# Kernel optimization log

Measured on AMD Instinct MI355X. Metric: run time of the kernel, lower is better.

Reference implementation:

```python
import jax, jax.numpy as jnp
import numpy as np

CAPACITY = 0.5


def setup_inputs() -> dict:
    key = jax.random.key(0)
    ks = jax.random.split(key, 5)
    B, L, D = 4, 4096, 1024
    Dff = 4 * D
    x = jax.random.normal(ks[0], (B, L, D), dtype=jnp.float32)
    w_router = jax.random.normal(ks[1], (D,), dtype=jnp.float32) / np.sqrt(D)
    w_bypass = jax.random.normal(ks[2], (D, D), dtype=jnp.float32) / np.sqrt(D)
    w1 = jax.random.normal(ks[3], (Dff, D), dtype=jnp.float32) / np.sqrt(D)
    w2 = jax.random.normal(ks[4], (D, Dff), dtype=jnp.float32) / np.sqrt(Dff)
    return {"x": x, "w_router": w_router, "w_bypass": w_bypass, "w1": w1, "w2": w2}


def _block_fn(x, w1, w2):
    # stand-in for the expensive full block: 2-layer GELU FFN (torch Linear: y = x W^T)
    h = jax.nn.gelu(jnp.einsum('bld,fd->blf', x, w1))
    return jnp.einsum('blf,df->bld', h, w2)


def reference(x, w_router, w_bypass, w1, w2):
    B, L, D = x.shape
    k = max(1, int(L * CAPACITY))  # static
    if k >= L:
        return _block_fn(x, w1, w2)
    # router scores (B, L)
    scores = jnp.einsum('bld,d->bl', x, w_router)
    _, top_idx = jax.lax.top_k(scores, k)          # (B, k)
    top_idx = jnp.sort(top_idx, axis=-1)           # (B, k), sorted positions
    # gather selected tokens -> (B, k, D)
    x_sel = jnp.take_along_axis(x, top_idx[:, :, None], axis=1)
    out_sel = _block_fn(x_sel, w1, w2)             # (B, k, D)
    # bypass path for all tokens
    output = jnp.einsum('bld,ed->ble', x, w_bypass)
    # scatter block outputs back onto selected positions
    b_idx = jnp.arange(B)[:, None]                 # (B, 1)
    output = output.at[b_idx, top_idx].set(out_sel)
    return output
```

## Files before the change

### kernel.cpp

```cpp
#include <hip/hip_runtime.h>
#include <stdint.h>
#include <math.h>


typedef __attribute__((ext_vector_type(8))) __bf16 bf16x8;
typedef __attribute__((ext_vector_type(4))) float f32x4;

__device__ __forceinline__ void async_cp16(const __bf16* g, __bf16* l) {
    __builtin_amdgcn_global_load_lds(
        (__attribute__((address_space(1))) void*)g,
        (__attribute__((address_space(3))) void*)l,
        16, 0, 0);
}

__device__ __forceinline__ float gelu_fast(float x) {
    float u = 1.5957691216057308f * x * (1.0f + 0.044715f * x * x);
    return x / (1.0f + __expf(-u));
}

__global__ __launch_bounds__(256) void router_cvt(
    const float* __restrict__ x, const float* __restrict__ wr,
    float* __restrict__ scores, __bf16* __restrict__ xb)
{
    int wid  = (blockIdx.x * blockDim.x + threadIdx.x) >> 6;
    int lane = threadIdx.x & 63;
    const float* row = x + (size_t)wid * 1024;
    __bf16* orow = xb + (size_t)wid * 1024;
    double s = 0.0;
    #pragma unroll
    for (int it = 0; it < 2; ++it) {
        int base = it * 512 + lane * 8;
        float4 a  = *(const float4*)(row + base);
        float4 b  = *(const float4*)(row + base + 4);
        float4 wa = *(const float4*)(wr + base);
        float4 wc = *(const float4*)(wr + base + 4);
        s += (double)a.x * wa.x + (double)a.y * wa.y
           + (double)a.z * wa.z + (double)a.w * wa.w
           + (double)b.x * wc.x + (double)b.y * wc.y
           + (double)b.z * wc.z + (double)b.w * wc.w;
        bf16x8 v;
        v[0] = (__bf16)a.x; v[1] = (__bf16)a.y; v[2] = (__bf16)a.z; v[3] = (__bf16)a.w;
        v[4] = (__bf16)b.x; v[5] = (__bf16)b.y; v[6] = (__bf16)b.z; v[7] = (__bf16)b.w;
        *(bf16x8*)(orow + base) = v;
    }
    #pragma unroll
    for (int off = 32; off > 0; off >>= 1) s += __shfl_down(s, off, 64);
    if (lane == 0) scores[wid] = (float)s;
}

__global__ __launch_bounds__(256) void cvt3(
    const float* __restrict__ p0, const float* __restrict__ p1,
    const float* __restrict__ p2,
    __bf16* __restrict__ o0, __bf16* __restrict__ o1, __bf16* __restrict__ o2,
    int c0, int c1, int c2)
{
    int chunk = blockIdx.x * 256 + threadIdx.x;
    const float* in; __bf16* out;
    if (chunk < c0)                { in = p0 + (size_t)chunk * 8;             out = o0 + (size_t)chunk * 8; }
    else if (chunk < c0 + c1)      { int c = chunk - c0;      in = p1 + (size_t)c * 8; out = o1 + (size_t)c * 8; }
    else if (chunk < c0 + c1 + c2) { int c = chunk - c0 - c1; in = p2 + (size_t)c * 8; out = o2 + (size_t)c * 8; }
    else return;
    float4 a = *(const float4*)(in);
    float4 b = *(const float4*)(in + 4);
    bf16x8 v;
    v[0] = (__bf16)a.x; v[1] = (__bf16)a.y; v[2] = (__bf16)a.z; v[3] = (__bf16)a.w;
    v[4] = (__bf16)b.x; v[5] = (__bf16)b.y; v[6] = (__bf16)b.z; v[7] = (__bf16)b.w;
    *(bf16x8*)(out) = v;
}

__global__ __launch_bounds__(1024) void topk_build(
    const float* __restrict__ scores,
    int* __restrict__ sel_rows, int* __restrict__ byp_rows)
{
    const int L = 4096, K = 2048;
    __shared__ unsigned long long key[4096];
    __shared__ int flag[4096];
    __shared__ int tsum[1024];
    int b = blockIdx.x, t = threadIdx.x;

    for (int i = t; i < L; i += 1024) {
        unsigned u = __float_as_uint(scores[b * L + i]);
        u = (u & 0x80000000u) ? ~u : (u | 0x80000000u);
        key[i] = ((unsigned long long)u << 32) | (unsigned)(L - 1 - i);
    }
    __syncthreads();

    for (int kk = 2; kk <= L; kk <<= 1) {
        for (int j = kk >> 1; j > 0; j >>= 1) {
            for (int i = t; i < L; i += 1024) {
                int p = i ^ j;
                if (p > i) {
                    unsigned long long a = key[i], c = key[p];
                    bool sw = ((i & kk) == 0) ? (a < c) : (a > c);
                    if (sw) { key[i] = c; key[p] = a; }
                }
            }
            __syncthreads();
        }
    }

    for (int s = t; s < L; s += 1024) {
        int idx = (L - 1) - (int)(key[s] & 0xffffffffu);
        flag[idx] = (s < K) ? 1 : 0;
    }
    __syncthreads();

    int base = t * 4;
    int f0 = flag[base], f1 = flag[base+1], f2 = flag[base+2], f3 = flag[base+3];
    tsum[t] = f0 + f1 + f2 + f3;
    __syncthreads();
    for (int off = 1; off < 1024; off <<= 1) {
        int v = tsum[t];
        if (t >= off) v += tsum[t - off];
        __syncthreads();
        tsum[t] = v;
        __syncthreads();
    }
    int run = (t > 0) ? tsum[t - 1] : 0;
    int fl[4] = {f0, f1, f2, f3};
    #pragma unroll
    for (int j = 0; j < 4; ++j) {
        int idx = base + j;
        if (fl[j]) { sel_rows[b * K + run] = b * L + idx; run++; }
        else       { byp_rows[b * (L - K) + (idx - run)] = b * L + idx; }
    }
}

template <bool GATHER_A, bool SCATTER_OUT, bool GELU_ACT, typename OT>
__global__ __launch_bounds__(256) void gemm_async(
    const __bf16* __restrict__ A, const __bf16* __restrict__ W,
    OT* __restrict__ Out, const int* __restrict__ rows,
    int K, int lda, int ldo)
{
    constexpr int BM = 128, BK = 64;
    __shared__ __align__(16) __bf16 As[BM * BK];
    __shared__ __align__(16) __bf16 Bs[BM * BK];
    __shared__ int rs[BM];

    const int tid = threadIdx.x;
    const int m0 = blockIdx.y * BM, n0 = blockIdx.x * BM;
    if (tid < BM) rs[tid] = rows ? rows[m0 + tid] : (m0 + tid);
    __syncthreads();

    const int sub = tid >> 3;
    const int gc  = (tid & 7) ^ (sub & 7);
    const __bf16* aptr[4]; const __bf16* bptr[4];
    __bf16* adst[4]; __bf16* bdst[4];
    #pragma unroll
    for (int i = 0; i < 4; ++i) {
        int row = i * 32 + sub;
        int ar  = GATHER_A ? rs[row] : (m0 + row);
        aptr[i] = A + (size_t)ar * lda + gc * 8;
        bptr[i] = W + (size_t)(n0 + row) * K + gc * 8;
        adst[i] = As + (i * 256 + tid) * 8;
        bdst[i] = Bs + (i * 256 + tid) * 8;
    }

    f32x4 acc[4][4] = {};
    const int lane = tid & 63;
    const int wv = tid >> 6;
    const int wr = (wv >> 1) * 64, wc = (wv & 1) * 64;
    const int r = lane & 15, quad = lane >> 4;

    for (int k0 = 0; k0 < K; k0 += BK) {
        #pragma unroll
        for (int i = 0; i < 4; ++i) async_cp16(aptr[i] + k0, adst[i]);
        #pragma unroll
        for (int i = 0; i < 4; ++i) async_cp16(bptr[i] + k0, bdst[i]);
        __syncthreads();

        #pragma unroll
        for (int ks = 0; ks < 2; ++ks) {
            bf16x8 af[4], bfm[4];
            #pragma unroll
            for (int mi = 0; mi < 4; ++mi) {
                int row = wr + mi * 16 + r;
                int swz = (ks * 4 + quad) ^ (row & 7);
                af[mi] = *(const bf16x8*)(As + row * BK + swz * 8);
            }
            #pragma unroll
            for (int ni = 0; ni < 4; ++ni) {
                int row = wc + ni * 16 + r;
                int swz = (ks * 4 + quad) ^ (row & 7);
                bfm[ni] = *(const bf16x8*)(Bs + row * BK + swz * 8);
            }
            #pragma unroll
            for (int mi = 0; mi < 4; ++mi)
                #pragma unroll
                for (int ni = 0; ni < 4; ++ni)
                    acc[mi][ni] = __builtin_amdgcn_mfma_f32_16x16x32_bf16(
                        af[mi], bfm[ni], acc[mi][ni], 0, 0, 0);
        }
        __syncthreads();
    }

    #pragma unroll
    for (int mi = 0; mi < 4; ++mi) {
        #pragma unroll
        for (int reg = 0; reg < 4; ++reg) {
            int rowl = wr + mi * 16 + quad * 4 + reg;
            int orow = SCATTER_OUT ? rs[rowl] : (m0 + rowl);
            OT* op = Out + (size_t)orow * ldo + n0;
            #pragma unroll
            for (int ni = 0; ni < 4; ++ni) {
                float v = acc[mi][ni][reg];
                if (GELU_ACT) v = gelu_fast(v);
                op[wc + ni * 16 + r] = (OT)v;
            }
        }
    }
}

__global__ __launch_bounds__(256) void gemm_tail(
    const __bf16* __restrict__ h, const __bf16* __restrict__ w2b,
    const __bf16* __restrict__ xb, const __bf16* __restrict__ wbb,
    float* __restrict__ Out,
    const int* __restrict__ sel_rows, const int* __restrict__ byp_rows)
{
    constexpr int BM = 128, BK = 64;
    __shared__ __align__(16) __bf16 As[BM * BK];
    __shared__ __align__(16) __bf16 Bs[BM * BK];
    __shared__ int rs[BM];

    const int z = blockIdx.z;
    const __bf16* A = z ? xb : h;
    const __bf16* W = z ? wbb : w2b;
    const int K = z ? 1024 : 4096;
    const int* rows = z ? byp_rows : sel_rows;
    const bool gat = (z != 0);

    const int tid = threadIdx.x;
    const int m0 = blockIdx.y * BM, n0 = blockIdx.x * BM;
    rs[tid & 127] = rows[m0 + (tid & 127)];
    __syncthreads();

    const int sub = tid >> 3;
    const int gc  = (tid & 7) ^ (sub & 7);
    const __bf16* aptr[4]; const __bf16* bptr[4];
    __bf16* adst[4]; __bf16* bdst[4];
    #pragma unroll
    for (int i = 0; i < 4; ++i) {
        int row = i * 32 + sub;
        int ar  = gat ? rs[row] : (m0 + row);
        aptr[i] = A + (size_t)ar * K + gc * 8;
        bptr[i] = W + (size_t)(n0 + row) * K + gc * 8;
        adst[i] = As + (i * 256 + tid) * 8;
        bdst[i] = Bs + (i * 256 + tid) * 8;
    }

    f32x4 acc[4][4] = {};
    const int lane = tid & 63;
    const int wv = tid >> 6;
    const int wrr = (wv >> 1) * 64, wc = (wv & 1) * 64;
    const int r = lane & 15, quad = lane >> 4;

    for (int k0 = 0; k0 < K; k0 += BK) {
        #pragma unroll
        for (int i = 0; i < 4; ++i) async_cp16(aptr[i] + k0, adst[i]);
        #pragma unroll
        for (int i = 0; i < 4; ++i) async_cp16(bptr[i] + k0, bdst[i]);
        __syncthreads();

        #pragma unroll
        for (int ks = 0; ks < 2; ++ks) {
            bf16x8 af[4], bfm[4];
            #pragma unroll
            for (int mi = 0; mi < 4; ++mi) {
                int row = wrr + mi * 16 + r;
                int swz = (ks * 4 + quad) ^ (row & 7);
                af[mi] = *(const bf16x8*)(As + row * BK + swz * 8);
            }
            #pragma unroll
            for (int ni = 0; ni < 4; ++ni) {
                int row = wc + ni * 16 + r;
                int swz = (ks * 4 + quad) ^ (row & 7);
                bfm[ni] = *(const bf16x8*)(Bs + row * BK + swz * 8);
            }
            #pragma unroll
            for (int mi = 0; mi < 4; ++mi)
                #pragma unroll
                for (int ni = 0; ni < 4; ++ni)
                    acc[mi][ni] = __builtin_amdgcn_mfma_f32_16x16x32_bf16(
                        af[mi], bfm[ni], acc[mi][ni], 0, 0, 0);
        }
        __syncthreads();
    }

    #pragma unroll
    for (int mi = 0; mi < 4; ++mi) {
        #pragma unroll
        for (int reg = 0; reg < 4; ++reg) {
            int rowl = wrr + mi * 16 + quad * 4 + reg;
            int orow = rs[rowl];
            float* op = Out + (size_t)orow * 1024 + n0;
            #pragma unroll
            for (int ni = 0; ni < 4; ++ni)
                op[wc + ni * 16 + r] = acc[mi][ni][reg];
        }
    }
}

extern "C" void kernel_launch(void* const* d_in, const int* in_sizes, int n_in,
                              void* d_out, int out_size, void* d_ws, size_t ws_size,
                              hipStream_t stream) {
    (void)in_sizes; (void)n_in; (void)out_size; (void)ws_size;
    const float* x  = (const float*)d_in[0];
    const float* wr = (const float*)d_in[1];
    const float* wb = (const float*)d_in[2];
    const float* w1 = (const float*)d_in[3];
    const float* w2 = (const float*)d_in[4];
    float* out = (float*)d_out;

    const int B = 4, L = 4096, D = 1024, DFF = 4096, KSEL = 2048;
    const int M = B * KSEL;
    const int NTOK = B * L;

    size_t n_x = (size_t)NTOK * D, n_wb = (size_t)D * D;
    size_t n_w1 = (size_t)DFF * D, n_w2 = (size_t)D * DFF;

    char* ws = (char*)d_ws;
    float* scores = (float*)ws;            ws += sizeof(float) * (size_t)NTOK;
    int* sel_rows = (int*)ws;              ws += sizeof(int) * (size_t)M;
    int* byp_rows = (int*)ws;              ws += sizeof(int) * (size_t)M;
    uintptr_t up = ((uintptr_t)ws + 255) & ~(uintptr_t)255;
    __bf16* xb  = (__bf16*)up;             up += 2 * n_x;
    __bf16* wbb = (__bf16*)up;             up += 2 * n_wb;
    __bf16* w1b = (__bf16*)up;             up += 2 * n_w1;
    __bf16* w2b = (__bf16*)up;             up += 2 * n_w2;
    up = (up + 255) & ~(uintptr_t)255;
    __bf16* h   = (__bf16*)up;

    router_cvt<<<NTOK / 4, 256, 0, stream>>>(x, wr, scores, xb);
    cvt3<<<(int)((n_wb + n_w1 + n_w2) / 8 / 256), 256, 0, stream>>>(
        wb, w1, w2, wbb, w1b, w2b,
        (int)(n_wb / 8), (int)(n_w1 / 8), (int)(n_w2 / 8));
    topk_build<<<B, 1024, 0, stream>>>(scores, sel_rows, byp_rows);

    gemm_async<true, false, true, __bf16>
        <<<dim3(DFF / 128, M / 128), 256, 0, stream>>>(
        xb, w1b, h, sel_rows, D, D, DFF);
    gemm_tail<<<dim3(D / 128, M / 128, 2), 256, 0, stream>>>(
        h, w2b, xb, wbb, out, sel_rows, byp_rows);
}
```

Measured before the change: 421.6 us.

## Replace bitonic top-k with radix select and remap GEMM tiles per XCD

The full 4096-element bitonic sort in shared memory is replaced by a 4-pass 8-bit radix select that finds the k-th score threshold, followed by two prefix scans that resolve ties and compact the selected and bypass rows. Separately, both GEMM kernels remap the linear block id so that consecutive groups of 8 blocks (one per XCD under round-robin dispatch) share an N tile while covering 8 different M tiles, aiming at better L2 reuse on MI355X. The radix select uses serial histogram scans on one thread and shared-memory atomics. The tile remap assumes gridDim.y is a multiple of 8.

```diff
diff --git a/kernel.cpp b/kernel.cpp
--- a/kernel.cpp
+++ b/kernel.cpp
@@ -73,57 +73,90 @@
     int* __restrict__ sel_rows, int* __restrict__ byp_rows)
 {
     const int L = 4096, K = 2048;
-    __shared__ unsigned long long key[4096];
-    __shared__ int flag[4096];
-    __shared__ int tsum[1024];
+    __shared__ unsigned u[4096];
+    __shared__ int hist[256];
+    __shared__ int scan_s[1024];
+    __shared__ unsigned s_pref;
+    __shared__ int s_kk;
     int b = blockIdx.x, t = threadIdx.x;
 
     for (int i = t; i < L; i += 1024) {
-        unsigned u = __float_as_uint(scores[b * L + i]);
-        u = (u & 0x80000000u) ? ~u : (u | 0x80000000u);
-        key[i] = ((unsigned long long)u << 32) | (unsigned)(L - 1 - i);
-    }
-    __syncthreads();
-
-    for (int kk = 2; kk <= L; kk <<= 1) {
-        for (int j = kk >> 1; j > 0; j >>= 1) {
-            for (int i = t; i < L; i += 1024) {
-                int p = i ^ j;
-                if (p > i) {
-                    unsigned long long a = key[i], c = key[p];
-                    bool sw = ((i & kk) == 0) ? (a < c) : (a > c);
-                    if (sw) { key[i] = c; key[p] = a; }
-                }
-            }
-            __syncthreads();
-        }
-    }
-
-    for (int s = t; s < L; s += 1024) {
-        int idx = (L - 1) - (int)(key[s] & 0xffffffffu);
-        flag[idx] = (s < K) ? 1 : 0;
-    }
-    __syncthreads();
+        unsigned v = __float_as_uint(scores[b * L + i]);
+        v = (v & 0x80000000u) ? ~v : (v | 0x80000000u);
+        u[i] = v;
+    }
+    if (t == 0) { s_pref = 0; s_kk = K; }
+    __syncthreads();
+
+    for (int shift = 24; shift >= 0; shift -= 8) {
+        if (t < 256) hist[t] = 0;
+        __syncthreads();
+        unsigned pref = s_pref;
+        for (int i = t; i < L; i += 1024) {
+            unsigned v = u[i];
+            bool in_set = (shift == 24) || ((v >> (shift + 8)) == pref);
+            if (in_set) atomicAdd(&hist[(v >> shift) & 255], 1);
+        }
+        __syncthreads();
+        if (t == 0) {
+            int kk = s_kk, cum = 0, bsel = 0;
+            for (int j = 255; j >= 0; --j) {
+                if (cum + hist[j] >= kk) { bsel = j; break; }
+                cum += hist[j];
+            }
+            s_kk = kk - cum;
+            s_pref = (pref << 8) | (unsigned)bsel;
+        }
+        __syncthreads();
+    }
+    unsigned thr = s_pref;
+    int need = s_kk;
 
     int base = t * 4;
-    int f0 = flag[base], f1 = flag[base+1], f2 = flag[base+2], f3 = flag[base+3];
-    tsum[t] = f0 + f1 + f2 + f3;
+    unsigned v0 = u[base], v1 = u[base+1], v2 = u[base+2], v3 = u[base+3];
+    int eq0 = (v0 == thr), eq1 = (v1 == thr), eq2 = (v2 == thr), eq3 = (v3 == thr);
+    scan_s[t] = eq0 + eq1 + eq2 + eq3;
     __syncthreads();
     for (int off = 1; off < 1024; off <<= 1) {
-        int v = tsum[t];
-        if (t >= off) v += tsum[t - off];
-        __syncthreads();
-        tsum[t] = v;
-        __syncthreads();
-    }
-    int run = (t > 0) ? tsum[t - 1] : 0;
-    int fl[4] = {f0, f1, f2, f3};
+        int v = scan_s[t];
+        if (t >= off) v += scan_s[t - off];
+        __syncthreads();
+        scan_s[t] = v;
+        __syncthreads();
+    }
+    int erun = (t > 0) ? scan_s[t - 1] : 0;
+    int sel[4];
+    {
+        int r = erun;
+        sel[0] = (v0 > thr) || (eq0 && r < need); r += eq0;
+        sel[1] = (v1 > thr) || (eq1 && r < need); r += eq1;
+        sel[2] = (v2 > thr) || (eq2 && r < need); r += eq2;
+        sel[3] = (v3 > thr) || (eq3 && r < need);
+    }
+    __syncthreads();
+
+    scan_s[t] = sel[0] + sel[1] + sel[2] + sel[3];
+    __syncthreads();
+    for (int off = 1; off < 1024; off <<= 1) {
+        int v = scan_s[t];
+        if (t >= off) v += scan_s[t - off];
+        __syncthreads();
+        scan_s[t] = v;
+        __syncthreads();
+    }
+    int run = (t > 0) ? scan_s[t - 1] : 0;
     #pragma unroll
     for (int j = 0; j < 4; ++j) {
         int idx = base + j;
-        if (fl[j]) { sel_rows[b * K + run] = b * L + idx; run++; }
-        else       { byp_rows[b * (L - K) + (idx - run)] = b * L + idx; }
-    }
+        if (sel[j]) { sel_rows[b * K + run] = b * L + idx; run++; }
+        else        { byp_rows[b * (L - K) + (idx - run)] = b * L + idx; }
+    }
+}
+
+__device__ __forceinline__ void xcd_map(int id, int nx, int& mt, int& nt) {
+    int grp = nx * 8;
+    mt = (id / grp) * 8 + (id & 7);
+    nt = (id % grp) >> 3;
 }
 
 template <bool GATHER_A, bool SCATTER_OUT, bool GELU_ACT, typename OT>
@@ -138,7 +171,9 @@
     __shared__ int rs[BM];
 
     const int tid = threadIdx.x;
-    const int m0 = blockIdx.y * BM, n0 = blockIdx.x * BM;
+    int mt, nt;
+    xcd_map(blockIdx.y * gridDim.x + blockIdx.x, gridDim.x, mt, nt);
+    const int m0 = mt * BM, n0 = nt * BM;
     if (tid < BM) rs[tid] = rows ? rows[m0 + tid] : (m0 + tid);
     __syncthreads();
 
@@ -230,7 +265,9 @@
     const bool gat = (z != 0);
 
     const int tid = threadIdx.x;
-    const int m0 = blockIdx.y * BM, n0 = blockIdx.x * BM;
+    int mt, nt;
+    xcd_map(blockIdx.y * gridDim.x + blockIdx.x, gridDim.x, mt, nt);
+    const int m0 = mt * BM, n0 = nt * BM;
     rs[tid & 127] = rows[m0 + (tid & 127)];
     __syncthreads();
 
```

Result: faster. 377.8 us (-10.4%).
